# Kernel optimization log

Measured on AMD Instinct MI355X. Metric: run time of the kernel, lower is better.

Reference implementation:

```python
import jax, jax.numpy as jnp
import numpy as np

NUM_NODES = 2048
NUM_OPS = 8
D, F, K = 64, 64, 64
H_NG = 128
H_EE = 64


def _make_edges(n):
    # edges[0]=i (src), edges[1]=j (dst) for i in [2,n), j in [0,i)
    src = np.concatenate([np.full(i, i, dtype=np.int64) for i in range(2, n)])
    dst = np.concatenate([np.arange(i, dtype=np.int64) for i in range(2, n)])
    return np.stack([src, dst])


def setup_inputs() -> dict:
    key = jax.random.key(0)
    ks = jax.random.split(key, 8)
    n = NUM_NODES
    s = lambda k, shape, fan_in: jax.random.normal(k, shape, jnp.float32) * (1.0 / np.sqrt(fan_in))
    return {
        "embed": jax.random.normal(ks[0], (n, D), jnp.float32),
        "W1": s(ks[1], (D, H_NG), D), "b1": jnp.zeros((H_NG,), jnp.float32),
        "W2": s(ks[2], (H_NG, H_NG), H_NG), "b2": jnp.zeros((H_NG,), jnp.float32),
        "W3": s(ks[3], (H_NG, F), H_NG), "b3": jnp.zeros((F,), jnp.float32),
        "We1": s(ks[4], (2 * F, H_EE), 2 * F), "be1": jnp.zeros((H_EE,), jnp.float32),
        "We2": s(ks[5], (H_EE, K), H_EE), "be2": jnp.zeros((K,), jnp.float32),
        "Wop": s(ks[6], (K, NUM_OPS), K), "bop": jnp.zeros((NUM_OPS,), jnp.float32),
        "edges": jnp.asarray(_make_edges(n)),
        "weights": jnp.ones((_make_edges(n).shape[1],), jnp.float32),
    }


def gcn_conv(x, W, b, src, dst, ew, n):
    # PyG GCNConv: x' = D^{-1/2} (A + I) D^{-1/2} (x W) + b, aggregated at dst
    h = x @ W
    loop = jnp.arange(n)
    src2 = jnp.concatenate([src, loop])
    dst2 = jnp.concatenate([dst, loop])
    w2 = jnp.concatenate([ew, jnp.ones((n,), x.dtype)])
    deg = jax.ops.segment_sum(w2, dst2, num_segments=n)
    dinv = jnp.where(deg > 0, jax.lax.rsqrt(deg), 0.0)
    norm = dinv[src2] * w2 * dinv[dst2]
    out = jax.ops.segment_sum(h[src2] * norm[:, None], dst2, num_segments=n)
    return out + b


def reference(embed, W1, b1, W2, b2, W3, b3, We1, be1, We2, be2, Wop, bop, edges, weights):
    n = embed.shape[0]
    src, dst = edges[0], edges[1]
    h = jax.nn.relu(gcn_conv(embed, W1, b1, src, dst, weights, n))
    h = jax.nn.relu(gcn_conv(h, W2, b2, src, dst, weights, n))
    h = jax.nn.relu(gcn_conv(h, W3, b3, src, dst, weights, n))  # [n, F]
    e = jnp.concatenate([h[src], h[dst]], axis=-1)              # [E, 2F]
    e = jax.nn.relu(e @ We1 + be1)
    e = jax.nn.relu(e @ We2 + be2)
    o = e @ Wop + bop                                            # [E, num_ops]
    p = jax.nn.softmax(o, axis=-1)
    # forward loop skips i == num_nodes-1; those rows of p remain zero
    mask = (src < n - 1)[:, None]
    return jnp.where(mask, p, 0.0)
```

## Files before the change

kernel.cpp:

```cpp
#include <hip/hip_runtime.h>
#include <math.h>

#define NN 2048
#define LASTN 2047

typedef __attribute__((ext_vector_type(8))) short short8;
typedef __attribute__((ext_vector_type(4))) float f32x4;
typedef __attribute__((ext_vector_type(4))) unsigned uint4v;

__device__ __forceinline__ float node_dinv(int j) {
  int deg = (j < 2) ? 2047 : (2048 - j);
  return rsqrtf((float)deg);
}

__device__ __forceinline__ void split_bf(float x, short& h, short& l) {
  unsigned u = __float_as_uint(x);
  unsigned r = u + 0x7FFFu + ((u >> 16) & 1u);
  h = (short)(r >> 16);
  float fh = __uint_as_float((r >> 16) << 16);
  float res = x - fh;
  unsigned u2 = __float_as_uint(res);
  unsigned r2 = u2 + 0x7FFFu + ((u2 >> 16) & 1u);
  l = (short)(r2 >> 16);
}

__device__ __forceinline__ unsigned cvt_pk_bf16(float a, float b) {
  unsigned r;
  asm("v_cvt_pk_bf16_f32 %0, %1, %2" : "=v"(r) : "v"(a), "v"(b));
  return r;
}

__device__ __forceinline__ void split_pair(float a, float b, unsigned& h, unsigned& l) {
  h = cvt_pk_bf16(a, b);
  float fa = __uint_as_float(h << 16);
  float fb = __uint_as_float(h & 0xFFFF0000u);
  l = cvt_pk_bf16(a - fa, b - fb);
}

__global__ __launch_bounds__(256) void prep(const float* __restrict__ embed,
                                            const float* __restrict__ We2,
                                            float* __restrict__ embedT,
                                            short* __restrict__ BfH,
                                            short* __restrict__ BfL) {
  __shared__ float tile[64][65];
  const int b = blockIdx.x;
  const int t = threadIdx.x;
  if (b < 32) {
    #pragma unroll
    for (int m = 0; m < 16; ++m) {
      int idx = m * 256 + t;
      int rl = idx >> 6, cc = idx & 63;
      tile[rl][cc] = embed[(b * 64 + rl) * 64 + cc];
    }
    __syncthreads();
    #pragma unroll
    for (int m = 0; m < 16; ++m) {
      int idx = m * 256 + t;
      int cc = idx >> 6, rl = idx & 63;
      embedT[cc * 2048 + b * 64 + rl] = tile[rl][cc];
    }
  } else {
    int tt = (b - 32) * 256 + t;
    int lane = tt & 63;
    int rest = tt >> 6;
    int ks = rest & 1;
    int ct = rest >> 1;
    int q = lane >> 4, l4 = lane & 15;
    int f = ct * 16 + l4;
    #pragma unroll
    for (int j = 0; j < 8; ++j) {
      int k = ks * 32 + q * 8 + j;
      float w = We2[k * 64 + f];
      short h, l;
      split_bf(w, h, l);
      int o = ((ct * 2 + ks) * 64 + lane) * 8 + j;
      BfH[o] = h;
      BfL[o] = l;
    }
  }
}

template <int K>
__global__ __launch_bounds__(512) void layer_fused(const float* __restrict__ XT,
                                                   const float* __restrict__ W,
                                                   const float* __restrict__ bias,
                                                   float* __restrict__ outT, int N) {
  const int c = blockIdx.x;
  const int t = threadIdx.x;
  __shared__ float wcol[K];
  __shared__ float sm[2048];
  __shared__ float part[512];
  if (t < K) wcol[t] = W[t * N + c];
  __syncthreads();
  float a0 = 0.f, a1 = 0.f, a2 = 0.f, a3 = 0.f;
  #pragma unroll 8
  for (int k = 0; k < K; ++k) {
    const float wk = wcol[k];
    const float* xr = XT + k * 2048 + t;
    a0 = fmaf(xr[0], wk, a0);
    a1 = fmaf(xr[512], wk, a1);
    a2 = fmaf(xr[1024], wk, a2);
    a3 = fmaf(xr[1536], wk, a3);
  }
  sm[t] = a0 * node_dinv(t);
  sm[t + 512] = a1 * node_dinv(t + 512);
  sm[t + 1024] = a2 * node_dinv(t + 1024);
  sm[t + 1536] = a3 * node_dinv(t + 1536);
  __syncthreads();
  const int j0 = 4 * t;
  float s0 = sm[j0], s1 = sm[j0 + 1], s2 = sm[j0 + 2], s3 = sm[j0 + 3];
  part[t] = (s0 + s1) + (s2 + s3);
  __syncthreads();
  for (int off = 1; off < 512; off <<= 1) {
    float v = part[t] + ((t + off < 512) ? part[t + off] : 0.f);
    __syncthreads();
    part[t] = v;
    __syncthreads();
  }
  float Q = (t < 511) ? part[t + 1] : 0.f;
  float Te3 = Q;
  float Te2 = Te3 + s3;
  float Te1 = Te2 + s2;
  float Te0 = Te1 + s1;
  const float bc = bias[c];
  float g0 = (j0 == 0) ? Te1 : Te0;
  float d0 = node_dinv(j0), d1 = node_dinv(j0 + 1);
  float d2 = node_dinv(j0 + 2), d3 = node_dinv(j0 + 3);
  float4 o;
  o.x = fmaxf(d0 * g0 + s0 * d0 + bc, 0.f);
  o.y = fmaxf(d1 * Te1 + s1 * d1 + bc, 0.f);
  o.z = fmaxf(d2 * Te2 + s2 * d2 + bc, 0.f);
  o.w = fmaxf(d3 * Te3 + s3 * d3 + bc, 0.f);
  *(float4*)(outT + (size_t)c * 2048 + j0) = o;
}

__global__ __launch_bounds__(256) void gemm_ab(const float* __restrict__ XT,
                                               const float* __restrict__ We1,
                                               const float* __restrict__ be1,
                                               float* __restrict__ A,
                                               float* __restrict__ B) {
  int idx = blockIdx.x * 256 + threadIdx.x;
  int r = idx >> 6, c = idx & 63;
  const float* WA = We1;
  const float* WB = We1 + 64 * 64;
  float a0 = 0.f, a1 = 0.f, b0 = 0.f, b1 = 0.f;
  for (int k = 0; k < 64; k += 2) {
    float x0 = XT[k * 2048 + r], x1 = XT[(k + 1) * 2048 + r];
    a0 = fmaf(x0, WA[k * 64 + c], a0);
    a1 = fmaf(x1, WA[(k + 1) * 64 + c], a1);
    b0 = fmaf(x0, WB[k * 64 + c], b0);
    b1 = fmaf(x1, WB[(k + 1) * 64 + c], b1);
  }
  A[idx] = a0 + a1 + be1[c];
  B[idx] = b0 + b1;
}

#define CHUNK 64
#define LSTR 68
#define EGY 2

__global__ __launch_bounds__(256, 4) void edge_mlp(const float* __restrict__ Amat,
                                                   const float* __restrict__ Bmat,
                                                   const short* __restrict__ BfH,
                                                   const short* __restrict__ BfL,
                                                   const float* __restrict__ be2,
                                                   const float* __restrict__ Wop,
                                                   const float* __restrict__ bop,
                                                   float* __restrict__ out) {
  const int i = LASTN - blockIdx.x;
  const long base = (long)i * (i - 1) / 2 - 1;
  const int tid = threadIdx.x;

  if (i == LASTN) {
    const float4 z = make_float4(0.f, 0.f, 0.f, 0.f);
    for (int j = blockIdx.y * 256 + tid; j < LASTN; j += EGY * 256) {
      size_t off = ((size_t)(base + j)) * 8;
      *(float4*)(out + off) = z;
      *(float4*)(out + off + 4) = z;
    }
    return;
  }

  int c = blockIdx.y;
  if (c * CHUNK >= i) return;

  __shared__ __align__(16) float sm[2][64 * LSTR];

  const int l = tid & 63, w = tid >> 6;
  const int l4 = l & 15, q = l >> 4;

  const float4* Arow = (const float4*)(Amat + (size_t)i * 64);
  const float4 a00 = Arow[q * 2], a01 = Arow[q * 2 + 1];
  const float4 a10 = Arow[8 + q * 2], a11 = Arow[8 + q * 2 + 1];

  short8 Bh[8], Bl[8];
  #pragma unroll
  for (int u = 0; u < 8; ++u) {
    Bh[u] = *(const short8*)(BfH + (u * 64 + l) * 8);
    Bl[u] = *(const short8*)(BfL + (u * 64 + l) * 8);
  }
  float bias[4];
  #pragma unroll
  for (int ct = 0; ct < 4; ++ct) bias[ct] = be2[ct * 16 + l4];

  auto stage_tile = [&](int cbase, int t, float* smb) {
    int j = cbase + t * 16 + l4;
    int jc = min(j, i - 1);
    const float4* Brow = (const float4*)(Bmat + (size_t)jc * 64);

    short8 ah[2], al[2];
    #pragma unroll
    for (int ks = 0; ks < 2; ++ks) {
      float4 bb0 = Brow[ks * 8 + q * 2];
      float4 bb1 = Brow[ks * 8 + q * 2 + 1];
      float4 aa0 = ks ? a10 : a00;
      float4 aa1 = ks ? a11 : a01;
      float v0 = fmaxf(aa0.x + bb0.x, 0.f), v1 = fmaxf(aa0.y + bb0.y, 0.f);
      float v2 = fmaxf(aa0.z + bb0.z, 0.f), v3 = fmaxf(aa0.w + bb0.w, 0.f);
      float v4 = fmaxf(aa1.x + bb1.x, 0.f), v5 = fmaxf(aa1.y + bb1.y, 0.f);
      float v6 = fmaxf(aa1.z + bb1.z, 0.f), v7 = fmaxf(aa1.w + bb1.w, 0.f);
      unsigned h0, h1, h2, h3, L0, L1, L2, L3;
      split_pair(v0, v1, h0, L0);
      split_pair(v2, v3, h1, L1);
      split_pair(v4, v5, h2, L2);
      split_pair(v6, v7, h3, L3);
      ah[ks] = __builtin_bit_cast(short8, (uint4v){h0, h1, h2, h3});
      al[ks] = __builtin_bit_cast(short8, (uint4v){L0, L1, L2, L3});
    }

    f32x4 acc[4];
    #pragma unroll
    for (int ct = 0; ct < 4; ++ct) acc[ct] = (f32x4){0.f, 0.f, 0.f, 0.f};
    #pragma unroll
    for (int ct = 0; ct < 4; ++ct)
      acc[ct] = __builtin_amdgcn_mfma_f32_16x16x32_bf16(ah[0], Bh[ct * 2 + 0], acc[ct], 0, 0, 0);
    #pragma unroll
    for (int ct = 0; ct < 4; ++ct)
      acc[ct] = __builtin_amdgcn_mfma_f32_16x16x32_bf16(ah[1], Bh[ct * 2 + 1], acc[ct], 0, 0, 0);
    #pragma unroll
    for (int ct = 0; ct < 4; ++ct)
      acc[ct] = __builtin_amdgcn_mfma_f32_16x16x32_bf16(ah[0], Bl[ct * 2 + 0], acc[ct], 0, 0, 0);
    #pragma unroll
    for (int ct = 0; ct < 4; ++ct)
      acc[ct] = __builtin_amdgcn_mfma_f32_16x16x32_bf16(ah[1], Bl[ct * 2 + 1], acc[ct], 0, 0, 0);
    #pragma unroll
    for (int ct = 0; ct < 4; ++ct)
      acc[ct] = __builtin_amdgcn_mfma_f32_16x16x32_bf16(al[0], Bh[ct * 2 + 0], acc[ct], 0, 0, 0);
    #pragma unroll
    for (int ct = 0; ct < 4; ++ct)
      acc[ct] = __builtin_amdgcn_mfma_f32_16x16x32_bf16(al[1], Bh[ct * 2 + 1], acc[ct], 0, 0, 0);

    #pragma unroll
    for (int ct = 0; ct < 4; ++ct) {
      int f = ct * 16 + l4;
      float4 st;
      st.x = fmaxf(acc[ct][0] + bias[ct], 0.f);
      st.y = fmaxf(acc[ct][1] + bias[ct], 0.f);
      st.z = fmaxf(acc[ct][2] + bias[ct], 0.f);
      st.w = fmaxf(acc[ct][3] + bias[ct], 0.f);
      *(float4*)(&smb[f * LSTR + t * 16 + q * 4]) = st;
    }
  };

  auto phase_b = [&](int cbase, const float* smb) {
    int j = cbase + l;
    float o0 = bop[0], o1 = bop[1], o2 = bop[2], o3 = bop[3];
    float o4 = bop[4], o5 = bop[5], o6 = bop[6], o7 = bop[7];
    #pragma unroll 8
    for (int f = 0; f < 64; ++f) {
      float v = smb[f * LSTR + l];
      o0 = fmaf(v, Wop[f * 8 + 0], o0);
      o1 = fmaf(v, Wop[f * 8 + 1], o1);
      o2 = fmaf(v, Wop[f * 8 + 2], o2);
      o3 = fmaf(v, Wop[f * 8 + 3], o3);
      o4 = fmaf(v, Wop[f * 8 + 4], o4);
      o5 = fmaf(v, Wop[f * 8 + 5], o5);
      o6 = fmaf(v, Wop[f * 8 + 6], o6);
      o7 = fmaf(v, Wop[f * 8 + 7], o7);
    }
    float mx = fmaxf(fmaxf(fmaxf(o0, o1), fmaxf(o2, o3)),
                     fmaxf(fmaxf(o4, o5), fmaxf(o6, o7)));
    float p0 = __expf(o0 - mx), p1 = __expf(o1 - mx), p2 = __expf(o2 - mx);
    float p3 = __expf(o3 - mx), p4 = __expf(o4 - mx), p5 = __expf(o5 - mx);
    float p6 = __expf(o6 - mx), p7 = __expf(o7 - mx);
    float rs = 1.0f / (((p0 + p1) + (p2 + p3)) + ((p4 + p5) + (p6 + p7)));
    if (j < i) {
      size_t off = ((size_t)(base + j)) * 8;
      *(float4*)(out + off) = make_float4(p0 * rs, p1 * rs, p2 * rs, p3 * rs);
      *(float4*)(out + off + 4) = make_float4(p4 * rs, p5 * rs, p6 * rs, p7 * rs);
    }
  };

  stage_tile(c * CHUNK, w, sm[0]);
  __syncthreads();

  int buf = 0, kc = 0;
  while (true) {
    const int wb = kc & 3;
    const int nc = c + EGY;
    if (nc * CHUNK < i) {
      int rel = (w - wb) & 3;
      if (rel == 1) {
        stage_tile(nc * CHUNK, 0, sm[buf ^ 1]);
      } else if (rel == 2) {
        stage_tile(nc * CHUNK, 1, sm[buf ^ 1]);
        stage_tile(nc * CHUNK, 2, sm[buf ^ 1]);
      } else if (rel == 3) {
        stage_tile(nc * CHUNK, 3, sm[buf ^ 1]);
      }
    }
    if (w == wb) phase_b(c * CHUNK, sm[buf]);
    __syncthreads();
    c = nc;
    ++kc;
    buf ^= 1;
    if (c * CHUNK >= i) break;
  }
}

extern "C" void kernel_launch(void* const* d_in, const int* in_sizes, int n_in,
                              void* d_out, int out_size, void* d_ws, size_t ws_size,
                              hipStream_t stream) {
  const float* embed = (const float*)d_in[0];
  const float* W1 = (const float*)d_in[1];
  const float* b1 = (const float*)d_in[2];
  const float* W2 = (const float*)d_in[3];
  const float* b2 = (const float*)d_in[4];
  const float* W3 = (const float*)d_in[5];
  const float* b3 = (const float*)d_in[6];
  const float* We1 = (const float*)d_in[7];
  const float* be1 = (const float*)d_in[8];
  const float* We2 = (const float*)d_in[9];
  const float* be2 = (const float*)d_in[10];
  const float* Wop = (const float*)d_in[11];
  const float* bop = (const float*)d_in[12];

  float* ws = (float*)d_ws;
  float* embedT = ws;
  float* h2T = ws;
  float* h1T = ws + 262144;
  float* Abuf = ws + 262144;
  float* Bbuf = ws + 393216;
  float* h3T = ws + 524288;
  short* BfH = (short*)(ws + 655360);
  short* BfL = (short*)(ws + 657408);
  float* outp = (float*)d_out;

  prep<<<34, 256, 0, stream>>>(embed, We2, embedT, BfH, BfL);
  layer_fused<64><<<128, 512, 0, stream>>>(embedT, W1, b1, h1T, 128);
  layer_fused<128><<<128, 512, 0, stream>>>(h1T, W2, b2, h2T, 128);
  layer_fused<128><<<64, 512, 0, stream>>>(h2T, W3, b3, h3T, 64);
  gemm_ab<<<512, 256, 0, stream>>>(h3T, We1, be1, Abuf, Bbuf);

  dim3 ge(2046, EGY, 1);
  edge_mlp<<<ge, 256, 0, stream>>>(Abuf, Bbuf, BfH, BfL, be2, Wop, bop, outp);
}
```

Baseline: 254.3 us.

## Make edge MLP warp-independent with register prefetch and swizzled LDS tiles

The edge MLP kernel changes from 256-thread blocks, where warps cooperatively stage tiles and rotate softmax duty under block barriers, to 128-thread blocks. In the new version each warp owns its own 64-edge chunk and its own LDS buffer, so no __syncthreads is needed. Bmat row loads are software-prefetched into registers one tile ahead and for the next chunk. The padded LDS stride is replaced by an XOR swizzle to avoid bank conflicts. This removes barrier stalls and the imbalance between staging and softmax work, at the cost of more registers per thread and a different occupancy and grid shape.

```diff
diff --git a/kernel.cpp b/kernel.cpp
--- a/kernel.cpp
+++ b/kernel.cpp
@@ -156,10 +156,9 @@
 }
 
 #define CHUNK 64
-#define LSTR 68
-#define EGY 2
-
-__global__ __launch_bounds__(256, 4) void edge_mlp(const float* __restrict__ Amat,
+#define EGY 4
+
+__global__ __launch_bounds__(128, 2) void edge_mlp(const float* __restrict__ Amat,
                                                    const float* __restrict__ Bmat,
                                                    const short* __restrict__ BfH,
                                                    const short* __restrict__ BfL,
@@ -173,7 +172,7 @@
 
   if (i == LASTN) {
     const float4 z = make_float4(0.f, 0.f, 0.f, 0.f);
-    for (int j = blockIdx.y * 256 + tid; j < LASTN; j += EGY * 256) {
+    for (int j = blockIdx.y * 128 + tid; j < LASTN; j += EGY * 128) {
       size_t off = ((size_t)(base + j)) * 8;
       *(float4*)(out + off) = z;
       *(float4*)(out + off + 4) = z;
@@ -181,12 +180,13 @@
     return;
   }
 
-  int c = blockIdx.y;
+  const int l = tid & 63, w = tid >> 6;
+  int c = blockIdx.y * 2 + w;
   if (c * CHUNK >= i) return;
 
-  __shared__ __align__(16) float sm[2][64 * LSTR];
-
-  const int l = tid & 63, w = tid >> 6;
+  __shared__ __align__(16) float sm[2][64 * 64];
+  float* smb = sm[w];
+
   const int l4 = l & 15, q = l >> 4;
 
   const float4* Arow = (const float4*)(Amat + (size_t)i * 64);
@@ -203,16 +203,24 @@
   #pragma unroll
   for (int ct = 0; ct < 4; ++ct) bias[ct] = be2[ct * 16 + l4];
 
-  auto stage_tile = [&](int cbase, int t, float* smb) {
+  const int wswz = (l4 & 7) << 2;
+
+  auto LOADT = [&](int cbase, int t, float4& b0, float4& b1, float4& b2, float4& b3) {
     int j = cbase + t * 16 + l4;
     int jc = min(j, i - 1);
     const float4* Brow = (const float4*)(Bmat + (size_t)jc * 64);
-
+    b0 = Brow[q * 2];
+    b1 = Brow[q * 2 + 1];
+    b2 = Brow[8 + q * 2];
+    b3 = Brow[8 + q * 2 + 1];
+  };
+
+  auto STAGE = [&](int t, float4 bb00, float4 bb01, float4 bb10, float4 bb11) {
     short8 ah[2], al[2];
     #pragma unroll
     for (int ks = 0; ks < 2; ++ks) {
-      float4 bb0 = Brow[ks * 8 + q * 2];
-      float4 bb1 = Brow[ks * 8 + q * 2 + 1];
+      float4 bb0 = ks ? bb10 : bb00;
+      float4 bb1 = ks ? bb11 : bb01;
       float4 aa0 = ks ? a10 : a00;
       float4 aa1 = ks ? a11 : a01;
       float v0 = fmaxf(aa0.x + bb0.x, 0.f), v1 = fmaxf(aa0.y + bb0.y, 0.f);
@@ -250,33 +258,36 @@
     for (int ct = 0; ct < 4; ++ct)
       acc[ct] = __builtin_amdgcn_mfma_f32_16x16x32_bf16(al[1], Bh[ct * 2 + 1], acc[ct], 0, 0, 0);
 
+    const int wcol = (t * 16 + q * 4) ^ wswz;
     #pragma unroll
     for (int ct = 0; ct < 4; ++ct) {
-      int f = ct * 16 + l4;
       float4 st;
       st.x = fmaxf(acc[ct][0] + bias[ct], 0.f);
       st.y = fmaxf(acc[ct][1] + bias[ct], 0.f);
       st.z = fmaxf(acc[ct][2] + bias[ct], 0.f);
       st.w = fmaxf(acc[ct][3] + bias[ct], 0.f);
-      *(float4*)(&smb[f * LSTR + t * 16 + q * 4]) = st;
+      *(float4*)(&smb[(ct * 16 + l4) * 64 + wcol]) = st;
     }
   };
 
-  auto phase_b = [&](int cbase, const float* smb) {
+  auto PHASEB = [&](int cbase) {
     int j = cbase + l;
     float o0 = bop[0], o1 = bop[1], o2 = bop[2], o3 = bop[3];
     float o4 = bop[4], o5 = bop[5], o6 = bop[6], o7 = bop[7];
-    #pragma unroll 8
-    for (int f = 0; f < 64; ++f) {
-      float v = smb[f * LSTR + l];
-      o0 = fmaf(v, Wop[f * 8 + 0], o0);
-      o1 = fmaf(v, Wop[f * 8 + 1], o1);
-      o2 = fmaf(v, Wop[f * 8 + 2], o2);
-      o3 = fmaf(v, Wop[f * 8 + 3], o3);
-      o4 = fmaf(v, Wop[f * 8 + 4], o4);
-      o5 = fmaf(v, Wop[f * 8 + 5], o5);
-      o6 = fmaf(v, Wop[f * 8 + 6], o6);
-      o7 = fmaf(v, Wop[f * 8 + 7], o7);
+    #pragma unroll
+    for (int fb = 0; fb < 64; fb += 8) {
+      #pragma unroll
+      for (int k = 0; k < 8; ++k) {
+        float v = smb[(fb + k) * 64 + (l ^ (k << 2))];
+        o0 = fmaf(v, Wop[(fb + k) * 8 + 0], o0);
+        o1 = fmaf(v, Wop[(fb + k) * 8 + 1], o1);
+        o2 = fmaf(v, Wop[(fb + k) * 8 + 2], o2);
+        o3 = fmaf(v, Wop[(fb + k) * 8 + 3], o3);
+        o4 = fmaf(v, Wop[(fb + k) * 8 + 4], o4);
+        o5 = fmaf(v, Wop[(fb + k) * 8 + 5], o5);
+        o6 = fmaf(v, Wop[(fb + k) * 8 + 6], o6);
+        o7 = fmaf(v, Wop[(fb + k) * 8 + 7], o7);
+      }
     }
     float mx = fmaxf(fmaxf(fmaxf(o0, o1), fmaxf(o2, o3)),
                      fmaxf(fmaxf(o4, o5), fmaxf(o6, o7)));
@@ -291,30 +302,26 @@
     }
   };
 
-  stage_tile(c * CHUNK, w, sm[0]);
-  __syncthreads();
-
-  int buf = 0, kc = 0;
+  float4 A0, A1, A2, A3, B0, B1, B2, B3;
+  LOADT(c * CHUNK, 0, A0, A1, A2, A3);
+  LOADT(c * CHUNK, 1, B0, B1, B2, B3);
   while (true) {
-    const int wb = kc & 3;
-    const int nc = c + EGY;
-    if (nc * CHUNK < i) {
-      int rel = (w - wb) & 3;
-      if (rel == 1) {
-        stage_tile(nc * CHUNK, 0, sm[buf ^ 1]);
-      } else if (rel == 2) {
-        stage_tile(nc * CHUNK, 1, sm[buf ^ 1]);
-        stage_tile(nc * CHUNK, 2, sm[buf ^ 1]);
-      } else if (rel == 3) {
-        stage_tile(nc * CHUNK, 3, sm[buf ^ 1]);
-      }
-    }
-    if (w == wb) phase_b(c * CHUNK, sm[buf]);
-    __syncthreads();
+    const int cb = c * CHUNK;
+    STAGE(0, A0, A1, A2, A3);
+    LOADT(cb, 2, A0, A1, A2, A3);
+    STAGE(1, B0, B1, B2, B3);
+    LOADT(cb, 3, B0, B1, B2, B3);
+    STAGE(2, A0, A1, A2, A3);
+    STAGE(3, B0, B1, B2, B3);
+    const int nc = c + 2 * EGY;
+    const bool more = (nc * CHUNK < i);
+    if (more) {
+      LOADT(nc * CHUNK, 0, A0, A1, A2, A3);
+      LOADT(nc * CHUNK, 1, B0, B1, B2, B3);
+    }
+    PHASEB(cb);
+    if (!more) break;
     c = nc;
-    ++kc;
-    buf ^= 1;
-    if (c * CHUNK >= i) break;
   }
 }
 
@@ -353,5 +360,5 @@
   gemm_ab<<<512, 256, 0, stream>>>(h3T, We1, be1, Abuf, Bbuf);
 
   dim3 ge(2046, EGY, 1);
-  edge_mlp<<<ge, 256, 0, stream>>>(Abuf, Bbuf, BfH, BfL, be2, Wop, bop, outp);
-}
+  edge_mlp<<<ge, 128, 0, stream>>>(Abuf, Bbuf, BfH, BfL, be2, Wop, bop, outp);
+}
```

After: 250.8 us. About the same (-1.4%).

## Fuse prep, GCN layers and edge projection into one cooperative kernel

Applied to the files above, without the earlier changes.

Replaces five separate launches (prep, three GCN layer kernels, and the A/B projection GEMM) with one cooperative kernel of 128 blocks that separates the stages with grid-wide syncs. Shared memory is now carved manually from one static buffer, and the projection GEMM is redistributed so each thread handles two outputs. The aim is to remove per-launch overhead and the idle gaps between the small dependent kernels. In exchange, every stage is limited to 128 blocks, which can reduce parallelism in the GEMM and prep phases, and each grid.sync adds its own cost.

```diff
diff --git a/kernel.cpp b/kernel.cpp
--- a/kernel.cpp
+++ b/kernel.cpp
@@ -1,5 +1,8 @@
 #include <hip/hip_runtime.h>
+#include <hip/hip_cooperative_groups.h>
 #include <math.h>
+
+namespace cg = cooperative_groups;
 
 #define NN 2048
 #define LASTN 2047
@@ -37,59 +40,16 @@
   l = cvt_pk_bf16(a - fa, b - fb);
 }
 
-__global__ __launch_bounds__(256) void prep(const float* __restrict__ embed,
-                                            const float* __restrict__ We2,
-                                            float* __restrict__ embedT,
-                                            short* __restrict__ BfH,
-                                            short* __restrict__ BfL) {
-  __shared__ float tile[64][65];
-  const int b = blockIdx.x;
-  const int t = threadIdx.x;
-  if (b < 32) {
-    #pragma unroll
-    for (int m = 0; m < 16; ++m) {
-      int idx = m * 256 + t;
-      int rl = idx >> 6, cc = idx & 63;
-      tile[rl][cc] = embed[(b * 64 + rl) * 64 + cc];
-    }
-    __syncthreads();
-    #pragma unroll
-    for (int m = 0; m < 16; ++m) {
-      int idx = m * 256 + t;
-      int cc = idx >> 6, rl = idx & 63;
-      embedT[cc * 2048 + b * 64 + rl] = tile[rl][cc];
-    }
-  } else {
-    int tt = (b - 32) * 256 + t;
-    int lane = tt & 63;
-    int rest = tt >> 6;
-    int ks = rest & 1;
-    int ct = rest >> 1;
-    int q = lane >> 4, l4 = lane & 15;
-    int f = ct * 16 + l4;
-    #pragma unroll
-    for (int j = 0; j < 8; ++j) {
-      int k = ks * 32 + q * 8 + j;
-      float w = We2[k * 64 + f];
-      short h, l;
-      split_bf(w, h, l);
-      int o = ((ct * 2 + ks) * 64 + lane) * 8 + j;
-      BfH[o] = h;
-      BfL[o] = l;
-    }
-  }
-}
-
-template <int K>
-__global__ __launch_bounds__(512) void layer_fused(const float* __restrict__ XT,
-                                                   const float* __restrict__ W,
-                                                   const float* __restrict__ bias,
-                                                   float* __restrict__ outT, int N) {
+__device__ __forceinline__ void layer_stage(const float* __restrict__ XT,
+                                            const float* __restrict__ W,
+                                            const float* __restrict__ bias,
+                                            float* __restrict__ outT,
+                                            int K, int N, float* smem) {
   const int c = blockIdx.x;
   const int t = threadIdx.x;
-  __shared__ float wcol[K];
-  __shared__ float sm[2048];
-  __shared__ float part[512];
+  float* wcol = smem;
+  float* sm = smem + 128;
+  float* part = smem + 2176;
   if (t < K) wcol[t] = W[t * N + c];
   __syncthreads();
   float a0 = 0.f, a1 = 0.f, a2 = 0.f, a3 = 0.f;
@@ -134,25 +94,91 @@
   *(float4*)(outT + (size_t)c * 2048 + j0) = o;
 }
 
-__global__ __launch_bounds__(256) void gemm_ab(const float* __restrict__ XT,
+__global__ __launch_bounds__(512) void gcn_all(const float* __restrict__ embed,
+                                               const float* __restrict__ We2,
+                                               const float* __restrict__ W1,
+                                               const float* __restrict__ b1,
+                                               const float* __restrict__ W2,
+                                               const float* __restrict__ b2,
+                                               const float* __restrict__ W3,
+                                               const float* __restrict__ b3,
                                                const float* __restrict__ We1,
                                                const float* __restrict__ be1,
-                                               float* __restrict__ A,
-                                               float* __restrict__ B) {
-  int idx = blockIdx.x * 256 + threadIdx.x;
-  int r = idx >> 6, c = idx & 63;
+                                               float* __restrict__ embedT,
+                                               float* __restrict__ h1T,
+                                               float* __restrict__ h2T,
+                                               float* __restrict__ h3T,
+                                               float* __restrict__ Abuf,
+                                               float* __restrict__ Bbuf,
+                                               short* __restrict__ BfH,
+                                               short* __restrict__ BfL) {
+  cg::grid_group grid = cg::this_grid();
+  __shared__ float smem[64 * 65];
+  const int t = threadIdx.x;
+
+  if (blockIdx.x < 32) {
+    const int b = blockIdx.x;
+    float(*tile)[65] = (float(*)[65])smem;
+    #pragma unroll
+    for (int m = 0; m < 8; ++m) {
+      int idx = m * 512 + t;
+      int rl = idx >> 6, cc = idx & 63;
+      tile[rl][cc] = embed[(b * 64 + rl) * 64 + cc];
+    }
+    __syncthreads();
+    #pragma unroll
+    for (int m = 0; m < 8; ++m) {
+      int idx = m * 512 + t;
+      int cc = idx >> 6, rl = idx & 63;
+      embedT[cc * 2048 + b * 64 + rl] = tile[rl][cc];
+    }
+  } else if (blockIdx.x == 32) {
+    int tt = t;
+    int lane = tt & 63;
+    int rest = tt >> 6;
+    int ks = rest & 1;
+    int ct = rest >> 1;
+    int q = lane >> 4, l4 = lane & 15;
+    int f = ct * 16 + l4;
+    #pragma unroll
+    for (int j = 0; j < 8; ++j) {
+      int k = ks * 32 + q * 8 + j;
+      float w = We2[k * 64 + f];
+      short h, l;
+      split_bf(w, h, l);
+      int o = ((ct * 2 + ks) * 64 + lane) * 8 + j;
+      BfH[o] = h;
+      BfL[o] = l;
+    }
+  }
+  grid.sync();
+
+  layer_stage(embedT, W1, b1, h1T, 64, 128, smem);
+  grid.sync();
+
+  layer_stage(h1T, W2, b2, h2T, 128, 128, smem);
+  grid.sync();
+
+  if (blockIdx.x < 64) layer_stage(h2T, W3, b3, h3T, 128, 64, smem);
+  grid.sync();
+
   const float* WA = We1;
   const float* WB = We1 + 64 * 64;
-  float a0 = 0.f, a1 = 0.f, b0 = 0.f, b1 = 0.f;
-  for (int k = 0; k < 64; k += 2) {
-    float x0 = XT[k * 2048 + r], x1 = XT[(k + 1) * 2048 + r];
-    a0 = fmaf(x0, WA[k * 64 + c], a0);
-    a1 = fmaf(x1, WA[(k + 1) * 64 + c], a1);
-    b0 = fmaf(x0, WB[k * 64 + c], b0);
-    b1 = fmaf(x1, WB[(k + 1) * 64 + c], b1);
-  }
-  A[idx] = a0 + a1 + be1[c];
-  B[idx] = b0 + b1;
+  #pragma unroll
+  for (int rep = 0; rep < 2; ++rep) {
+    int idx = rep * 65536 + blockIdx.x * 512 + t;
+    int r = idx >> 6, c = idx & 63;
+    float a0 = 0.f, a1 = 0.f, b0 = 0.f, b1 = 0.f;
+    for (int k = 0; k < 64; k += 2) {
+      float x0 = h3T[k * 2048 + r], x1 = h3T[(k + 1) * 2048 + r];
+      a0 = fmaf(x0, WA[k * 64 + c], a0);
+      a1 = fmaf(x1, WA[(k + 1) * 64 + c], a1);
+      b0 = fmaf(x0, WB[k * 64 + c], b0);
+      b1 = fmaf(x1, WB[(k + 1) * 64 + c], b1);
+    }
+    Abuf[idx] = a0 + a1 + be1[c];
+    Bbuf[idx] = b0 + b1;
+  }
 }
 
 #define CHUNK 64
@@ -252,13 +278,12 @@
 
     #pragma unroll
     for (int ct = 0; ct < 4; ++ct) {
-      int f = ct * 16 + l4;
       float4 st;
       st.x = fmaxf(acc[ct][0] + bias[ct], 0.f);
       st.y = fmaxf(acc[ct][1] + bias[ct], 0.f);
       st.z = fmaxf(acc[ct][2] + bias[ct], 0.f);
       st.w = fmaxf(acc[ct][3] + bias[ct], 0.f);
-      *(float4*)(&smb[f * LSTR + t * 16 + q * 4]) = st;
+      *(float4*)(&smb[(ct * 16 + l4) * LSTR + t * 16 + q * 4]) = st;
     }
   };
 
@@ -346,11 +371,10 @@
   short* BfL = (short*)(ws + 657408);
   float* outp = (float*)d_out;
 
-  prep<<<34, 256, 0, stream>>>(embed, We2, embedT, BfH, BfL);
-  layer_fused<64><<<128, 512, 0, stream>>>(embedT, W1, b1, h1T, 128);
-  layer_fused<128><<<128, 512, 0, stream>>>(h1T, W2, b2, h2T, 128);
-  layer_fused<128><<<64, 512, 0, stream>>>(h2T, W3, b3, h3T, 64);
-  gemm_ab<<<512, 256, 0, stream>>>(h3T, We1, be1, Abuf, Bbuf);
+  void* args[] = {&embed, &We2, &W1, &b1, &W2, &b2, &W3, &b3, &We1, &be1,
+                  &embedT, &h1T, &h2T, &h3T, &Abuf, &Bbuf, &BfH, &BfL};
+  hipLaunchCooperativeKernel((void*)gcn_all, dim3(128), dim3(512), args, 0,
+                             stream);
 
   dim3 ge(2046, EGY, 1);
   edge_mlp<<<ge, 256, 0, stream>>>(Abuf, Bbuf, BfH, BfL, be2, Wop, bop, outp);
```

Result: slower. 340.7 us (+34.0%).
